# Performance work log

Hardware: AMD Instinct MI355X
Metric: run time of the kernel (lower is better)

Reference implementation:

```python
import jax, jax.numpy as jnp
import numpy as np

DIM = 256
NUM_HEADS = 8
HEAD_DIM = DIM // NUM_HEADS


def setup_inputs() -> dict:
    key = jax.random.key(0)
    k_x, k_wq, k_bq, k_wp, k_bp = jax.random.split(key, 5)
    x = jax.random.normal(k_x, (4, DIM, 64, 64), dtype=jnp.float32)
    # 1x1 convs == per-pixel linear layers over channels
    w_qkv = jax.random.normal(k_wq, (3 * DIM, DIM), dtype=jnp.float32) * (DIM ** -0.5)
    b_qkv = jax.random.normal(k_bq, (3 * DIM,), dtype=jnp.float32) * 0.02
    w_proj = jax.random.normal(k_wp, (DIM, DIM), dtype=jnp.float32) * (DIM ** -0.5)
    b_proj = jax.random.normal(k_bp, (DIM,), dtype=jnp.float32) * 0.02
    return {"x": x, "w_qkv": w_qkv, "b_qkv": b_qkv, "w_proj": w_proj, "b_proj": b_proj}


def reference(x, w_qkv, b_qkv, w_proj, b_proj):
    B, C, H, W = x.shape
    S = H * W
    h, d = NUM_HEADS, HEAD_DIM
    # flatten spatial dims: (B, C, H, W) -> (B, S, C)
    xf = x.reshape(B, C, S).transpose(0, 2, 1)
    # 1x1 conv qkv: (B, S, 3C)
    qkv = xf @ w_qkv.T + b_qkv
    q, k, v = jnp.split(qkv, 3, axis=-1)
    # channel dim splits as (heads, head_dim): (B, S, C) -> (B, h, S, d)
    split = lambda t: t.reshape(B, S, h, d).transpose(0, 2, 1, 3)
    q, k, v = split(q), split(k), split(v)
    scale = d ** -0.5
    attn = jnp.einsum('bhsd,bhtd->bhst', q, k) * scale  # (B, h, S, S)
    attn = jax.nn.softmax(attn, axis=-1)
    out = jnp.einsum('bhst,bhtd->bhsd', attn, v)
    # merge heads: (B, h, S, d) -> (B, S, C)
    out = out.transpose(0, 2, 1, 3).reshape(B, S, C)
    out = out @ w_proj.T + b_proj
    # back to (B, C, H, W)
    return out.transpose(0, 2, 1).reshape(B, C, H, W)
```

## Files before the change

kernel.cpp:

```cpp
#include <hip/hip_runtime.h>


typedef __attribute__((ext_vector_type(8))) short short8;
typedef __attribute__((ext_vector_type(4))) float f4;

__device__ __forceinline__ short f2bs(float f) {
  union { float f; unsigned u; } v; v.f = f;
  unsigned r = v.u + 0x7FFFu + ((v.u >> 16) & 1u);
  return (short)(r >> 16);
}

__device__ __forceinline__ short8 cvt8(f4 a, f4 b) {
  short8 o;
  o[0] = f2bs(a[0]); o[1] = f2bs(a[1]); o[2] = f2bs(a[2]); o[3] = f2bs(a[3]);
  o[4] = f2bs(b[0]); o[5] = f2bs(b[1]); o[6] = f2bs(b[2]); o[7] = f2bs(b[3]);
  return o;
}

__device__ __forceinline__ int pkhu(float lo, float hi) {
  union { float f; unsigned u; } a, b; a.f = lo; b.f = hi;
  return (int)__builtin_amdgcn_perm(b.u + 0x8000u, a.u + 0x8000u, 0x07060302u);
}

__global__ __launch_bounds__(256) void k_qkv(
    const float* __restrict__ x, const float* __restrict__ w,
    const float* __restrict__ bias,
    short* __restrict__ Qr, short* __restrict__ Kq, short* __restrict__ Vt) {
  const int tid = threadIdx.x;
  const int L = tid & 63, wv = tid >> 6;
  const int ln15 = L & 15, quad = L >> 4;
  const int mt = blockIdx.x;
  const int b = mt >> 6;
  const int s0 = (mt & 63) << 6;
  const int j0 = blockIdx.y << 6;
  const int jw = j0 + wv * 16;

  __shared__ __align__(16) short tl[4 * 64 * 16];

  f4 acc[4] = {{0,0,0,0},{0,0,0,0},{0,0,0,0},{0,0,0,0}};
  const float* wb = w + (jw + ln15) * 256 + quad * 8;
  const float* xb = x + b * (256 * 4096) + s0 + ln15;

#pragma unroll 2
  for (int cb = 0; cb < 256; cb += 32) {
    f4 a0 = *(const f4*)(wb + cb);
    f4 a1 = *(const f4*)(wb + cb + 4);
    short8 af = cvt8(a0, a1);
    const float* xc = xb + (cb + quad * 8) * 4096;
#pragma unroll
    for (int sub = 0; sub < 4; ++sub) {
      const float* xs = xc + sub * 16;
      short8 bf;
#pragma unroll
      for (int jj = 0; jj < 8; ++jj) bf[jj] = f2bs(xs[jj * 4096]);
      acc[sub] = __builtin_amdgcn_mfma_f32_16x16x32_bf16(af, bf, acc[sub], 0, 0, 0);
    }
  }

  float bj[4];
#pragma unroll
  for (int r = 0; r < 4; ++r) bj[r] = bias[jw + quad * 4 + r];

  const int type = j0 >> 8;
  if (type == 2) {
    const int jv = jw - 512;
    const int h = jv >> 5;
    const int dbase = jv & 31;
#pragma unroll
    for (int r = 0; r < 4; ++r) {
      const int d = dbase + quad * 4 + r;
      short* vp = Vt + (size_t)((b * 8 + h) * 32 + d) * 4096 + s0 + ln15;
#pragma unroll
      for (int sub = 0; sub < 4; ++sub)
        vp[sub * 16] = f2bs(acc[sub][r] + bj[r]);
    }
  } else {
    const float qsc = 0.17677669529663689f * 1.44269504088896f;
    const float mul = (type == 0) ? qsc : 1.0f;
    short* dst = (type == 0) ? Qr : Kq;
    const int hj = jw & 255;
    short* tw = tl + wv * 1024;
#pragma unroll
    for (int sub = 0; sub < 4; ++sub) {
      const int s = sub * 16 + ln15;
      const int swz = (s >> 2) & 1;
#pragma unroll
      for (int r = 0; r < 4; ++r) {
        const int dl = quad * 4 + r;
        tw[s * 16 + (((dl >> 3) ^ swz) * 8) + (dl & 7)] = f2bs((acc[sub][r] + bj[r]) * mul);
      }
    }
    const int h = hj >> 5;
    const int d0 = hj & 31;
#pragma unroll
    for (int i = 0; i < 2; ++i) {
      const int sl = i * 32 + (L >> 1);
      const int gg = L & 1;
      const int g2 = gg ^ ((sl >> 2) & 1);
      short8 row = *(const short8*)(tw + sl * 16 + g2 * 8);
      *(short8*)(dst + (size_t)((b * 8 + h) * 4096 + s0 + sl) * 32 + d0 + gg * 8) = row;
    }
  }
}

__global__ __launch_bounds__(256, 8) void k_attn(
    const short* __restrict__ Qr, const short* __restrict__ Kq,
    const short* __restrict__ Vt, short* __restrict__ O) {
  const int tid = threadIdx.x;
  const int L = tid & 63, wv = tid >> 6;
  const int ln15 = L & 15, quad = L >> 4;
  const int bh = blockIdx.y;
  const int b = bh >> 3, h = bh & 7;
  const int qt = wv & 1, half = wv >> 1;
  const int qb = blockIdx.x * 64 + qt * 32;

  const short* Qb = Qr + (size_t)bh * 4096 * 32;
  const short* Kb = Kq + (size_t)bh * 4096 * 32 + half * 2048 * 32;
  const short* Vb = Vt + (size_t)bh * 32 * 4096 + half * 2048;

  __shared__ __align__(16) short plds[4][2048];
  __shared__ float l_up[2][32];
  short* pw = plds[wv];
  const int sw = ln15 & 14;

  short8 qf[2];
#pragma unroll
  for (int qs = 0; qs < 2; ++qs)
    qf[qs] = *(const short8*)(Qb + (qb + qs * 16 + ln15) * 32 + quad * 8);

  f4 acc[2][2] = {{{0,0,0,0},{0,0,0,0}},{{0,0,0,0},{0,0,0,0}}};
  float lsum[2] = {0.f, 0.f};
  const f4 z4 = {0.f, 0.f, 0.f, 0.f};

  const short* kp = Kb + ln15 * 32 + quad * 8;
  const short* vp = Vb + ln15 * 4096 + quad * 8;

  for (int kb = 0; kb < 2048; kb += 64) {
#pragma unroll
    for (int t = 0; t < 4; ++t) {
      short8 kf = *(const short8*)(kp + (kb + t * 16) * 32);
#pragma unroll
      for (int qs = 0; qs < 2; ++qs) {
        f4 sc = __builtin_amdgcn_mfma_f32_16x16x32_bf16(kf, qf[qs], z4, 0, 0, 0);
        float p0 = __builtin_amdgcn_exp2f(sc[0]);
        float p1 = __builtin_amdgcn_exp2f(sc[1]);
        float p2 = __builtin_amdgcn_exp2f(sc[2]);
        float p3 = __builtin_amdgcn_exp2f(sc[3]);
        lsum[qs] += (p0 + p1) + (p2 + p3);
        int2 pr;
        pr.x = pkhu(p0, p1);
        pr.y = pkhu(p2, p3);
        const int gw = ((t << 2) + quad) ^ sw;
        *(int2*)(pw + qs * 1024 + ln15 * 64 + gw * 4) = pr;
      }
    }
#pragma unroll
    for (int ks = 0; ks < 2; ++ks) {
      short8 vf0 = *(const short8*)(vp + kb + ks * 32);
      short8 vf1 = *(const short8*)(vp + 16 * 4096 + kb + ks * 32);
#pragma unroll
      for (int qs = 0; qs < 2; ++qs) {
        const int g0 = ((ks << 3) + (quad << 1)) ^ sw;
        short8 pf = *(const short8*)(pw + qs * 1024 + ln15 * 64 + g0 * 4);
        acc[qs][0] = __builtin_amdgcn_mfma_f32_16x16x32_bf16(pf, vf0, acc[qs][0], 0, 0, 0);
        acc[qs][1] = __builtin_amdgcn_mfma_f32_16x16x32_bf16(pf, vf1, acc[qs][1], 0, 0, 0);
      }
    }
  }

  float lfull[2];
#pragma unroll
  for (int qs = 0; qs < 2; ++qs) {
    float l = lsum[qs];
    l += __shfl_xor(l, 16);
    l += __shfl_xor(l, 32);
    lfull[qs] = l;
  }

  if (half == 1) {
    float* cw = (float*)plds[wv];
#pragma unroll
    for (int qs = 0; qs < 2; ++qs) {
#pragma unroll
      for (int dg = 0; dg < 2; ++dg)
#pragma unroll
        for (int r = 0; r < 4; ++r)
          cw[(qs * 16 + quad * 4 + r) * 32 + dg * 16 + ln15] = acc[qs][dg][r];
      if (quad == 0) l_up[qt][qs * 16 + ln15] = lfull[qs];
    }
  }
  __syncthreads();
  if (half == 0) {
    const float* cu = (const float*)plds[wv + 2];
#pragma unroll
    for (int qs = 0; qs < 2; ++qs) {
#pragma unroll
      for (int r = 0; r < 4; ++r) {
        const float lown = __shfl(lfull[qs], quad * 4 + r);
        const float lup = l_up[qt][qs * 16 + quad * 4 + r];
        const float rl = 1.0f / (lown + lup);
        const int sg = qb + qs * 16 + quad * 4 + r;
        short* op = O + (size_t)(b * 4096 + sg) * 256 + h * 32 + ln15;
        const int ci = (qs * 16 + quad * 4 + r) * 32 + ln15;
        op[0]  = f2bs((acc[qs][0][r] + cu[ci]) * rl);
        op[16] = f2bs((acc[qs][1][r] + cu[ci + 16]) * rl);
      }
    }
  }
}

__global__ __launch_bounds__(256) void k_proj(
    const short* __restrict__ O, const float* __restrict__ w,
    const float* __restrict__ bias, float* __restrict__ out) {
  const int tid = threadIdx.x;
  const int L = tid & 63, wv = tid >> 6;
  const int ln15 = L & 15, quad = L >> 4;
  const int m0 = blockIdx.x * 64 + wv * 16;
  const int n0 = blockIdx.y << 6;
  const int b = m0 >> 12, s0 = m0 & 4095;

  f4 acc[4] = {{0,0,0,0},{0,0,0,0},{0,0,0,0},{0,0,0,0}};
  const short* Ob = O + (size_t)(m0 + ln15) * 256 + quad * 8;
  const float* wb = w + (n0 + ln15) * 256 + quad * 8;

#pragma unroll 2
  for (int cb = 0; cb < 256; cb += 32) {
    short8 af = *(const short8*)(Ob + cb);
#pragma unroll
    for (int sub = 0; sub < 4; ++sub) {
      f4 b0 = *(const f4*)(wb + sub * (16 * 256) + cb);
      f4 b1 = *(const f4*)(wb + sub * (16 * 256) + cb + 4);
      short8 bf = cvt8(b0, b1);
      acc[sub] = __builtin_amdgcn_mfma_f32_16x16x32_bf16(af, bf, acc[sub], 0, 0, 0);
    }
  }

  __shared__ float tl[4][64 * 17];
  float* tw = tl[wv];
#pragma unroll
  for (int sub = 0; sub < 4; ++sub) {
    const float bv = bias[n0 + sub * 16 + ln15];
#pragma unroll
    for (int r = 0; r < 4; ++r)
      tw[(sub * 16 + ln15) * 17 + quad * 4 + r] = acc[sub][r] + bv;
  }
#pragma unroll
  for (int i = 0; i < 4; ++i) {
    const int c = i * 16 + (L >> 2);
    const int ms = (L & 3) * 4;
    f4 v;
#pragma unroll
    for (int j = 0; j < 4; ++j) v[j] = tw[c * 17 + ms + j];
    *(f4*)(out + (size_t)b * (256 * 4096) + (size_t)(n0 + c) * 4096 + s0 + ms) = v;
  }
}

extern "C" void kernel_launch(void* const* d_in, const int* in_sizes, int n_in,
                              void* d_out, int out_size, void* d_ws, size_t ws_size,
                              hipStream_t stream) {
  const float* x      = (const float*)d_in[0];
  const float* w_qkv  = (const float*)d_in[1];
  const float* b_qkv  = (const float*)d_in[2];
  const float* w_proj = (const float*)d_in[3];
  const float* b_proj = (const float*)d_in[4];
  float* out = (float*)d_out;

  const size_t SEG = (size_t)4 * 8 * 4096 * 32;
  short* Qr = (short*)d_ws;
  short* Kq = Qr + SEG;
  short* Vt = Kq + SEG;
  short* O  = Vt + SEG;

  k_qkv <<<dim3(256, 12), 256, 0, stream>>>(x, w_qkv, b_qkv, Qr, Kq, Vt);
  k_attn<<<dim3(64, 32),  256, 0, stream>>>(Qr, Kq, Vt, O);
  k_proj<<<dim3(256, 4),  256, 0, stream>>>(O, w_proj, b_proj, out);
}
```

Baseline: 329.8 us.

## Keep softmax P in registers via permlane swaps and compute row sums with MFMA

```diff
diff --git a/kernel.cpp b/kernel.cpp
--- a/kernel.cpp
+++ b/kernel.cpp
@@ -15,11 +15,6 @@
   o[0] = f2bs(a[0]); o[1] = f2bs(a[1]); o[2] = f2bs(a[2]); o[3] = f2bs(a[3]);
   o[4] = f2bs(b[0]); o[5] = f2bs(b[1]); o[6] = f2bs(b[2]); o[7] = f2bs(b[3]);
   return o;
-}
-
-__device__ __forceinline__ int pkhu(float lo, float hi) {
-  union { float f; unsigned u; } a, b; a.f = lo; b.f = hi;
-  return (int)__builtin_amdgcn_perm(b.u + 0x8000u, a.u + 0x8000u, 0x07060302u);
 }
 
 __global__ __launch_bounds__(256) void k_qkv(
@@ -103,7 +98,7 @@
   }
 }
 
-__global__ __launch_bounds__(256, 8) void k_attn(
+__global__ __launch_bounds__(256, 5) void k_attn(
     const short* __restrict__ Qr, const short* __restrict__ Kq,
     const short* __restrict__ Vt, short* __restrict__ O) {
   const int tid = threadIdx.x;
@@ -118,90 +113,96 @@
   const short* Kb = Kq + (size_t)bh * 4096 * 32 + half * 2048 * 32;
   const short* Vb = Vt + (size_t)bh * 32 * 4096 + half * 2048;
 
-  __shared__ __align__(16) short plds[4][2048];
+  __shared__ float cbuf[2][32 * 33];
   __shared__ float l_up[2][32];
-  short* pw = plds[wv];
-  const int sw = ln15 & 14;
 
   short8 qf[2];
 #pragma unroll
   for (int qs = 0; qs < 2; ++qs)
     qf[qs] = *(const short8*)(Qb + (qb + qs * 16 + ln15) * 32 + quad * 8);
 
+  short8 ones;
+#pragma unroll
+  for (int j = 0; j < 8; ++j) ones[j] = (short)0x3F80;
+
   f4 acc[2][2] = {{{0,0,0,0},{0,0,0,0}},{{0,0,0,0},{0,0,0,0}}};
-  float lsum[2] = {0.f, 0.f};
+  f4 accl[2] = {{0,0,0,0},{0,0,0,0}};
   const f4 z4 = {0.f, 0.f, 0.f, 0.f};
 
   const short* kp = Kb + ln15 * 32 + quad * 8;
   const short* vp = Vb + ln15 * 4096 + quad * 8;
 
   for (int kb = 0; kb < 2048; kb += 64) {
-#pragma unroll
-    for (int t = 0; t < 4; ++t) {
-      short8 kf = *(const short8*)(kp + (kb + t * 16) * 32);
-#pragma unroll
-      for (int qs = 0; qs < 2; ++qs) {
+    short8 vf[2][2];
+#pragma unroll
+    for (int f = 0; f < 2; ++f)
+#pragma unroll
+      for (int dg = 0; dg < 2; ++dg)
+        vf[f][dg] = *(const short8*)(vp + dg * (16 * 4096) + kb + f * 32);
+
+#pragma unroll
+    for (int qs = 0; qs < 2; ++qs) {
+      int dwa[4][2];
+#pragma unroll
+      for (int t = 0; t < 4; ++t) {
+        short8 kf = *(const short8*)(kp + (kb + t * 16) * 32);
         f4 sc = __builtin_amdgcn_mfma_f32_16x16x32_bf16(kf, qf[qs], z4, 0, 0, 0);
         float p0 = __builtin_amdgcn_exp2f(sc[0]);
         float p1 = __builtin_amdgcn_exp2f(sc[1]);
         float p2 = __builtin_amdgcn_exp2f(sc[2]);
         float p3 = __builtin_amdgcn_exp2f(sc[3]);
-        lsum[qs] += (p0 + p1) + (p2 + p3);
-        int2 pr;
-        pr.x = pkhu(p0, p1);
-        pr.y = pkhu(p2, p3);
-        const int gw = ((t << 2) + quad) ^ sw;
-        *(int2*)(pw + qs * 1024 + ln15 * 64 + gw * 4) = pr;
-      }
-    }
-#pragma unroll
-    for (int ks = 0; ks < 2; ++ks) {
-      short8 vf0 = *(const short8*)(vp + kb + ks * 32);
-      short8 vf1 = *(const short8*)(vp + 16 * 4096 + kb + ks * 32);
-#pragma unroll
-      for (int qs = 0; qs < 2; ++qs) {
-        const int g0 = ((ks << 3) + (quad << 1)) ^ sw;
-        short8 pf = *(const short8*)(pw + qs * 1024 + ln15 * 64 + g0 * 4);
-        acc[qs][0] = __builtin_amdgcn_mfma_f32_16x16x32_bf16(pf, vf0, acc[qs][0], 0, 0, 0);
-        acc[qs][1] = __builtin_amdgcn_mfma_f32_16x16x32_bf16(pf, vf1, acc[qs][1], 0, 0, 0);
-      }
-    }
-  }
-
-  float lfull[2];
-#pragma unroll
-  for (int qs = 0; qs < 2; ++qs) {
-    float l = lsum[qs];
-    l += __shfl_xor(l, 16);
-    l += __shfl_xor(l, 32);
-    lfull[qs] = l;
+        asm("v_cvt_pk_bf16_f32 %0, %1, %2" : "=v"(dwa[t][0]) : "v"(p0), "v"(p1));
+        asm("v_cvt_pk_bf16_f32 %0, %1, %2" : "=v"(dwa[t][1]) : "v"(p2), "v"(p3));
+      }
+      union { int i[4]; short8 s; } pk[2];
+#pragma unroll
+      for (int f = 0; f < 2; ++f)
+#pragma unroll
+        for (int u = 0; u < 2; ++u) {
+          int a = dwa[2 * f][u];
+          int c = dwa[2 * f + 1][u];
+          asm("v_permlane32_swap_b32 %0, %1" : "+v"(a), "+v"(c));
+          asm("v_permlane16_swap_b32 %0, %1" : "+v"(a), "+v"(c));
+          pk[f].i[u] = a;
+          pk[f].i[u + 2] = c;
+        }
+      accl[qs] = __builtin_amdgcn_mfma_f32_16x16x32_bf16(pk[0].s, ones, accl[qs], 0, 0, 0);
+      accl[qs] = __builtin_amdgcn_mfma_f32_16x16x32_bf16(pk[1].s, ones, accl[qs], 0, 0, 0);
+      acc[qs][0] = __builtin_amdgcn_mfma_f32_16x16x32_bf16(pk[0].s, vf[0][0], acc[qs][0], 0, 0, 0);
+      acc[qs][1] = __builtin_amdgcn_mfma_f32_16x16x32_bf16(pk[0].s, vf[0][1], acc[qs][1], 0, 0, 0);
+      acc[qs][0] = __builtin_amdgcn_mfma_f32_16x16x32_bf16(pk[1].s, vf[1][0], acc[qs][0], 0, 0, 0);
+      acc[qs][1] = __builtin_amdgcn_mfma_f32_16x16x32_bf16(pk[1].s, vf[1][1], acc[qs][1], 0, 0, 0);
+    }
   }
 
   if (half == 1) {
-    float* cw = (float*)plds[wv];
+    float* cw = cbuf[qt];
 #pragma unroll
     for (int qs = 0; qs < 2; ++qs) {
 #pragma unroll
       for (int dg = 0; dg < 2; ++dg)
 #pragma unroll
         for (int r = 0; r < 4; ++r)
-          cw[(qs * 16 + quad * 4 + r) * 32 + dg * 16 + ln15] = acc[qs][dg][r];
-      if (quad == 0) l_up[qt][qs * 16 + ln15] = lfull[qs];
+          cw[(qs * 16 + quad * 4 + r) * 33 + dg * 16 + ln15] = acc[qs][dg][r];
+      if (ln15 == 0) {
+#pragma unroll
+        for (int r = 0; r < 4; ++r)
+          l_up[qt][qs * 16 + quad * 4 + r] = accl[qs][r];
+      }
     }
   }
   __syncthreads();
   if (half == 0) {
-    const float* cu = (const float*)plds[wv + 2];
+    const float* cu = cbuf[qt];
 #pragma unroll
     for (int qs = 0; qs < 2; ++qs) {
 #pragma unroll
       for (int r = 0; r < 4; ++r) {
-        const float lown = __shfl(lfull[qs], quad * 4 + r);
         const float lup = l_up[qt][qs * 16 + quad * 4 + r];
-        const float rl = 1.0f / (lown + lup);
+        const float rl = 1.0f / (accl[qs][r] + lup);
         const int sg = qb + qs * 16 + quad * 4 + r;
         short* op = O + (size_t)(b * 4096 + sg) * 256 + h * 32 + ln15;
-        const int ci = (qs * 16 + quad * 4 + r) * 32 + ln15;
+        const int ci = (qs * 16 + quad * 4 + r) * 33 + ln15;
         op[0]  = f2bs((acc[qs][0][r] + cu[ci]) * rl);
         op[16] = f2bs((acc[qs][1][r] + cu[ci + 16]) * rl);
       }
```

Result: no change. 325.0 us (-1.5%).
